# Optimization experiments

Hardware: AMD Instinct MI355X
Metric: run time of the kernel (lower is better)

Reference implementation:

```python
import jax, jax.numpy as jnp
import numpy as np

D1, D2 = 64, 64          # degree1, degree2
BW1, BW2 = 3, 3          # bandwidths
WIDTH = 64


def dst_mat(n):
    # Orthonormal DST-I matrix: self-inverse, stand-in for sp.WSWA / sp.sin_transform.
    k = np.arange(1, n + 1)
    M = np.sqrt(2.0 / (n + 1)) * np.sin(np.pi * np.outer(k, k) / (n + 1))
    return jnp.asarray(M, jnp.float32)


def transform2d(x, S_row, S_col):
    # apply spectral transform along last axis then axis -2 (T_pipe with axes [-1,-2])
    x = jnp.einsum('bcij,jk->bcik', x, S_col)
    return jnp.einsum('ki,bcij->bckj', S_row, x)


def wswano(u, w, out_ch):
    # WSWANO.forward: transform -> quasi-diag (unfold+einsum) multiply -> zero-pad -> inverse transform
    B, C, Nx, Ny = u.shape
    S1, S2 = dst_mat(Ny), dst_mat(Nx)
    a = transform2d(u, S2, S1)
    ap = a[:, :, :D1 + BW1 - 1, :D2 + BW2 - 1]
    # torch.nn.Unfold(kernel=(bw1,bw2)): patches ordered (c, ki, kj) x row-major positions
    patches = jnp.stack([ap[:, :, i:i + D1, j:j + D2]
                         for i in range(BW1) for j in range(BW2)], axis=2)  # [B,C,bw1*bw2,D1,D2]
    xp = patches.reshape(B, C * BW1 * BW2, D1 * D2)
    out = jnp.einsum('bix,iox->box', xp, w)  # quasi-diagonal spectral multiply
    b = jnp.zeros((B, out_ch, Nx, Ny), u.dtype).at[:, :, :D1, :D2].set(
        out.reshape(B, out_ch, D1, D2))
    return transform2d(b, S2, S1)  # DST-I is self-inverse => iT_pipe


def conv1x1(x, w, b):
    return jnp.einsum('bchw,oc->bohw', x, w) + b[None, :, None, None]


def gelu(x):
    return jax.nn.gelu(x, approximate=False)


def setup_inputs():
    key = jax.random.key(0)
    ks = jax.random.split(key, 18)
    B, Nx, Ny, W = 16, 128, 128, WIDTH

    def cw(k, cin, cout):
        return (2.0 / (cin + cout)) * jax.random.uniform(
            k, (cin * BW1 * BW2, cout, D1 * D2), jnp.float32)

    return {
        'x': jax.random.normal(ks[0], (B, Nx, Ny, 3), jnp.float32),
        'convl_w': cw(ks[1], 3, W - 3),
        'conv0_w': cw(ks[2], W, W),
        'conv1_w': cw(ks[3], W, W),
        'conv2_w': cw(ks[4], W, W),
        'conv3_w': cw(ks[5], W, W),
        'w0_w': 0.02 * jax.random.normal(ks[6], (W, W), jnp.float32),
        'w0_b': 0.02 * jax.random.normal(ks[7], (W,), jnp.float32),
        'w1_w': 0.02 * jax.random.normal(ks[8], (W, W), jnp.float32),
        'w1_b': 0.02 * jax.random.normal(ks[9], (W,), jnp.float32),
        'w2_w': 0.02 * jax.random.normal(ks[10], (W, W), jnp.float32),
        'w2_b': 0.02 * jax.random.normal(ks[11], (W,), jnp.float32),
        'w3_w': 0.02 * jax.random.normal(ks[12], (W, W), jnp.float32),
        'w3_b': 0.02 * jax.random.normal(ks[13], (W,), jnp.float32),
        'fc1_w': 0.02 * jax.random.normal(ks[14], (W, 128), jnp.float32),
        'fc1_b': 0.02 * jax.random.normal(ks[15], (128,), jnp.float32),
        'fc2_w': 0.02 * jax.random.normal(ks[16], (128, 1), jnp.float32),
        'fc2_b': 0.02 * jax.random.normal(ks[17], (1,), jnp.float32),
    }


def reference(x, convl_w, conv0_w, conv1_w, conv2_w, conv3_w,
              w0_w, w0_b, w1_w, w1_b, w2_w, w2_b, w3_w, w3_b,
              fc1_w, fc1_b, fc2_w, fc2_b):
    x = jnp.transpose(x, (0, 3, 1, 2))                       # [B,3,Nx,Ny]
    x = jnp.concatenate([x, gelu(wswano(x, convl_w, WIDTH - 3))], axis=1)
    for ww, wb, cw_ in ((w0_w, w0_b, conv0_w), (w1_w, w1_b, conv1_w),
                        (w2_w, w2_b, conv2_w), (w3_w, w3_b, conv3_w)):
        x = x + gelu(conv1x1(x, ww, wb) + wswano(x, cw_, WIDTH))  # skip + GELU block
    x = jnp.transpose(x, (0, 2, 3, 1))                       # [B,Nx,Ny,width]
    x = gelu(x @ fc1_w + fc1_b)
    return x @ fc2_w + fc2_b                                  # [B,Nx,Ny,1]
```

## Files before the change

kernel.cpp:

```cpp
#include <hip/hip_runtime.h>
#include <math.h>

#define NB 16
#define NN 128
#define WC 64
#define DD 64
#define NP 66

typedef float v4f __attribute__((ext_vector_type(4)));
typedef unsigned int u32;

__device__ __forceinline__ float gelu_f(float x) {
    return 0.5f * x * (1.0f + erff(x * 0.70710678118654752f));
}

__device__ __forceinline__ void gload16(const float* g, float* l) {
    __builtin_amdgcn_global_load_lds(
        (const __attribute__((address_space(1))) u32*)g,
        (__attribute__((address_space(3))) u32*)l, 16, 0, 0);
}

__global__ void k_dst(float* __restrict__ S) {
    int idx = blockIdx.x * 256 + threadIdx.x;
    int k = idx >> 7, j = idx & 127;
    double arg = 3.14159265358979323846 * (double)((k + 1) * (j + 1)) / 129.0;
    S[idx] = (float)(sqrt(2.0 / 129.0) * sin(arg));
}

__global__ void k_tin(const float* __restrict__ in, float* __restrict__ xc) {
    int idx = blockIdx.x * 256 + threadIdx.x;
    int j = idx & 127;
    int i = (idx >> 7) & 127;
    int t = idx >> 14;
    int b = t / 3, c = t - b * 3;
    xc[(((size_t)b * WC + c) << 14) + i * 128 + j] =
        in[((size_t)(b * 128 + i) * 128 + j) * 3 + c];
}

__global__ __launch_bounds__(256) void k_tfwd66(const float* __restrict__ Xg,
                                                float* __restrict__ Yc,
                                                const float* __restrict__ Sg,
                                                int Cact) {
    __shared__ float sSt[80 * 132];
    __shared__ float sU[66 * 132];
    int bid = blockIdx.x;
    int b = bid / Cact, c = bid - b * Cact;
    const float* X = Xg + (((size_t)b * WC + c) << 14);
    int tid = threadIdx.x;
    int tx = tid & 15, ty = tid >> 4;
    for (int l = tid; l < 80 * 128; l += 256)
        sSt[(l >> 7) * 132 + (l & 127)] = Sg[l];
    float acc[8][5];
#pragma unroll
    for (int r = 0; r < 8; ++r)
#pragma unroll
        for (int q = 0; q < 5; ++q) acc[r][q] = 0.f;
    for (int jh = 0; jh < 2; ++jh) {
        __syncthreads();
        for (int l = tid; l < 8192; l += 256)
            sU[(l >> 6) * 68 + (l & 63)] = X[((l >> 6) << 7) + jh * 64 + (l & 63)];
        __syncthreads();
        for (int jj = 0; jj < 64; jj += 4) {
            float4 xv[8], sv[5];
#pragma unroll
            for (int r = 0; r < 8; ++r)
                xv[r] = *(const float4*)&sU[(ty + 16 * r) * 68 + jj];
#pragma unroll
            for (int q = 0; q < 5; ++q)
                sv[q] = *(const float4*)&sSt[(tx + 16 * q) * 132 + jh * 64 + jj];
#pragma unroll
            for (int r = 0; r < 8; ++r)
#pragma unroll
                for (int q = 0; q < 5; ++q) {
                    acc[r][q] += xv[r].x * sv[q].x;
                    acc[r][q] += xv[r].y * sv[q].y;
                    acc[r][q] += xv[r].z * sv[q].z;
                    acc[r][q] += xv[r].w * sv[q].w;
                }
        }
    }
    __syncthreads();
#pragma unroll
    for (int q = 0; q < 5; ++q) {
        int k = tx + 16 * q;
        if (k < 66) {
#pragma unroll
            for (int r = 0; r < 8; ++r)
                sU[k * 132 + ty + 16 * r] = acc[r][q];
        }
    }
    __syncthreads();
    float a2[5][5];
#pragma unroll
    for (int r = 0; r < 5; ++r)
#pragma unroll
        for (int q = 0; q < 5; ++q) a2[r][q] = 0.f;
    for (int i0 = 0; i0 < 128; i0 += 4) {
        float4 sv[5], tv[5];
#pragma unroll
        for (int r = 0; r < 5; ++r)
            sv[r] = *(const float4*)&sSt[(ty + 16 * r) * 132 + i0];
#pragma unroll
        for (int q = 0; q < 5; ++q) {
            int m = tx + 16 * q;
            if (m < 66) tv[q] = *(const float4*)&sU[m * 132 + i0];
            else { tv[q].x = 0.f; tv[q].y = 0.f; tv[q].z = 0.f; tv[q].w = 0.f; }
        }
#pragma unroll
        for (int r = 0; r < 5; ++r)
#pragma unroll
            for (int q = 0; q < 5; ++q) {
                a2[r][q] += sv[r].x * tv[q].x;
                a2[r][q] += sv[r].y * tv[q].y;
                a2[r][q] += sv[r].z * tv[q].z;
                a2[r][q] += sv[r].w * tv[q].w;
            }
    }
    float* Y = Yc + (size_t)(b * WC + c) * 4488;
#pragma unroll
    for (int r = 0; r < 5; ++r) {
        int kk = ty + 16 * r;
        if (kk < 66) {
#pragma unroll
            for (int q = 0; q < 5; ++q) {
                int m = tx + 16 * q;
                if (m < 66) Y[kk * 68 + m] = a2[r][q];
            }
        }
    }
}

__global__ __launch_bounds__(256, 3) void k_tinv(const float* __restrict__ Op,
                                                 float* __restrict__ Yg,
                                                 const float* __restrict__ Sg,
                                                 int Cact, int ncc, int ch_off, int do_gelu) {
    __shared__ float sS[64 * 64];
    __shared__ float sXT[64 * 132];
    int bid = blockIdx.x;
    int b = bid / Cact, c = bid - b * Cact;
    const float* X = Op + ((size_t)(b * WC + c) << 12);
    const size_t cstride = (size_t)NB * WC * 4096;
    float* Y = Yg + (((size_t)b * WC + c + ch_off) << 14);
    int tid = threadIdx.x;
    for (int l = tid; l < 4096; l += 256)
        sS[l] = Sg[((l >> 6) << 7) + (l & 63)];
    for (int l = tid; l < 4096; l += 256) {
        int r = l >> 6, q = l & 63;
        float v = X[l];
        for (int cc = 1; cc < ncc; ++cc) v += X[cc * cstride + l];
        sXT[r * 66 + q] = v;
    }
    __syncthreads();
    int cg = tid & 7;
    int rg = tid >> 3;
    v4f aP[2][2], aM[2][2];
#pragma unroll
    for (int r = 0; r < 2; ++r)
#pragma unroll
        for (int m = 0; m < 2; ++m) {
            aP[r][m].x = 0.f; aP[r][m].y = 0.f; aP[r][m].z = 0.f; aP[r][m].w = 0.f;
            aM[r][m].x = 0.f; aM[r][m].y = 0.f; aM[r][m].z = 0.f; aM[r][m].w = 0.f;
        }
    for (int jp = 0; jp < 32; ++jp) {
        float2 x0 = *(const float2*)&sXT[(rg * 2 + 0) * 66 + 2 * jp];
        float2 x1 = *(const float2*)&sXT[(rg * 2 + 1) * 66 + 2 * jp];
#pragma unroll
        for (int m = 0; m < 2; ++m) {
            v4f se = *(const v4f*)&sS[(2 * jp) * 64 + cg * 4 + 32 * m];
            v4f so = *(const v4f*)&sS[(2 * jp + 1) * 64 + cg * 4 + 32 * m];
            aP[0][m] += se * x0.x;  aM[0][m] += so * x0.y;
            aP[1][m] += se * x1.x;  aM[1][m] += so * x1.y;
        }
    }
    __syncthreads();
#pragma unroll
    for (int r = 0; r < 2; ++r)
#pragma unroll
        for (int m = 0; m < 2; ++m) {
            v4f tlo = aP[r][m] + aM[r][m];
            v4f td  = aP[r][m] - aM[r][m];
            v4f thi; thi.x = td.w; thi.y = td.z; thi.z = td.y; thi.w = td.x;
            int row = rg * 2 + r;
            *(v4f*)&sXT[row * 132 + cg * 4 + 32 * m] = tlo;
            *(v4f*)&sXT[row * 132 + 124 - cg * 4 - 32 * m] = thi;
        }
    __syncthreads();
    v4f p2[2][4], m2[2][4];
#pragma unroll
    for (int r = 0; r < 2; ++r)
#pragma unroll
        for (int m = 0; m < 4; ++m) {
            p2[r][m].x = 0.f; p2[r][m].y = 0.f; p2[r][m].z = 0.f; p2[r][m].w = 0.f;
            m2[r][m].x = 0.f; m2[r][m].y = 0.f; m2[r][m].z = 0.f; m2[r][m].w = 0.f;
        }
    for (int ip = 0; ip < 32; ++ip) {
        float2 sve = *(const float2*)&sS[(2 * ip) * 64 + rg * 2];
        float2 svo = *(const float2*)&sS[(2 * ip + 1) * 64 + rg * 2];
#pragma unroll
        for (int m = 0; m < 4; ++m) {
            v4f te = *(const v4f*)&sXT[(2 * ip) * 132 + cg * 4 + 32 * m];
            v4f to = *(const v4f*)&sXT[(2 * ip + 1) * 132 + cg * 4 + 32 * m];
            p2[0][m] += te * sve.x;  p2[1][m] += te * sve.y;
            m2[0][m] += to * svo.x;  m2[1][m] += to * svo.y;
        }
    }
#pragma unroll
    for (int r = 0; r < 2; ++r) {
        int rlo = rg * 2 + r, rhi = 127 - rlo;
#pragma unroll
        for (int m = 0; m < 4; ++m) {
            v4f ylo = p2[r][m] + m2[r][m];
            v4f yhi = p2[r][m] - m2[r][m];
            if (do_gelu) {
                ylo.x = gelu_f(ylo.x); ylo.y = gelu_f(ylo.y);
                ylo.z = gelu_f(ylo.z); ylo.w = gelu_f(ylo.w);
                yhi.x = gelu_f(yhi.x); yhi.y = gelu_f(yhi.y);
                yhi.z = gelu_f(yhi.z); yhi.w = gelu_f(yhi.w);
            }
            *(v4f*)&Y[rlo * 128 + cg * 4 + 32 * m] = ylo;
            *(v4f*)&Y[rhi * 128 + cg * 4 + 32 * m] = yhi;
        }
    }
}

__global__ __launch_bounds__(256, 2) void k_mix6(const float* __restrict__ Ac,
                                                 const float* __restrict__ Wt,
                                                 float* __restrict__ Op,
                                                 int Cin, int Cout, int cper) {
    __shared__ __align__(16) float sa[2][16 * 4 * 68];
    int bx = blockIdx.x;
    int ocb = blockIdx.y;
    int ccb = blockIdx.z;
    int c0 = ccb * cper;
    int c1 = c0 + cper; if (c1 > Cin) c1 = Cin;
    int tid = threadIdx.x;
    int ocl = tid & 7, yq = (tid >> 3) & 15, xh = tid >> 7;
    int x = bx * 2 + xh;
    int oc = ocb * 8 + ocl;
    bool ocok = oc < Cout;
    v4f z4; z4.x = 0.f; z4.y = 0.f; z4.z = 0.f; z4.w = 0.f;

    const size_t wstep = (size_t)Cout * 4096;
    const float* wbase = Wt + (size_t)(ocok ? oc : 0) * 4096 + x * 64 + (yq << 2);

    int gbase[5];
#pragma unroll
    for (int k = 0; k < 5; ++k) {
        int f = 4 * tid + 1024 * k;
        int fv = (f < 4352) ? f : 0;
        int bb = fv / 272; int off = fv - bb * 272;
        gbase[k] = bb * (WC * 4488) + bx * 136 + off;
    }

    float acc[16][4];
#pragma unroll
    for (int bb = 0; bb < 16; ++bb)
#pragma unroll
        for (int k = 0; k < 4; ++k) acc[bb][k] = 0.f;

    {
        const float* src = Ac + (size_t)c0 * 4488;
#pragma unroll
        for (int k = 0; k < 4; ++k)
            gload16(src + gbase[k], &sa[0][4 * tid + 1024 * k]);
        if (tid < 64) gload16(src + gbase[4], &sa[0][4 * tid + 4096]);
    }
    v4f wvA[9];
#pragma unroll
    for (int t = 0; t < 9; ++t)
        wvA[t] = ocok ? __builtin_nontemporal_load(
                            (const v4f*)(wbase + ((size_t)c0 * 9 + t) * wstep))
                      : z4;
    __syncthreads();

    int cur = 0;
    for (int c = c0; c < c1; ++c) {
        bool hn = (c + 1) < c1;
        v4f wvN[9];
        if (hn) {
            float* dst = sa[cur ^ 1];
            const float* src = Ac + (size_t)(c + 1) * 4488;
#pragma unroll
            for (int k = 0; k < 4; ++k)
                gload16(src + gbase[k], dst + 4 * tid + 1024 * k);
            if (tid < 64) gload16(src + gbase[4], dst + 4 * tid + 4096);
#pragma unroll
            for (int t = 0; t < 9; ++t)
                wvN[t] = ocok ? __builtin_nontemporal_load(
                                    (const v4f*)(wbase + ((size_t)(c + 1) * 9 + t) * wstep))
                              : z4;
        }
        const float* sab = sa[cur];
#pragma unroll
        for (int pi = 0; pi < 3; ++pi) {
#pragma unroll
            for (int bb = 0; bb < 16; ++bb) {
                const float* sp = &sab[(bb * 4 + xh + pi) * 68 + (yq << 2)];
                float4 s0 = *(const float4*)sp;
                float2 s1 = *(const float2*)(sp + 4);
                float sv[6] = {s0.x, s0.y, s0.z, s0.w, s1.x, s1.y};
#pragma unroll
                for (int k = 0; k < 4; ++k)
#pragma unroll
                    for (int pj = 0; pj < 3; ++pj)
                        acc[bb][k] = fmaf(sv[k + pj], wvA[pi * 3 + pj][k], acc[bb][k]);
            }
        }
        if (hn) {
            __syncthreads();
#pragma unroll
            for (int t = 0; t < 9; ++t) wvA[t] = wvN[t];
            cur ^= 1;
        }
    }

    if (ocok) {
        float* Opc = Op + (size_t)ccb * ((size_t)NB * WC * 4096);
#pragma unroll
        for (int bb = 0; bb < 16; ++bb) {
            float4 o4;
            o4.x = acc[bb][0]; o4.y = acc[bb][1];
            o4.z = acc[bb][2]; o4.w = acc[bb][3];
            *(float4*)&Opc[(((size_t)bb * WC + oc) << 12) + x * 64 + (yq << 2)] = o4;
        }
    }
}

__global__ __launch_bounds__(256) void k_blockup(float* __restrict__ xc,
                                                 const float* __restrict__ sp,
                                                 const float* __restrict__ wmat,
                                                 const float* __restrict__ bias) {
    __shared__ float sw[64 * 64];
    __shared__ float sx[128 * 65];
    __shared__ float sb[64];
    int bi = blockIdx.x;
    int b = bi >> 7, i = bi & 127;
    int tid = threadIdx.x;
    for (int l = tid; l < 4096; l += 256) sw[l] = wmat[l];
    if (tid < 64) sb[tid] = bias[tid];
    for (int l = tid; l < 8192; l += 256) {
        int c = l >> 7, j = l & 127;
        sx[j * 65 + c] = xc[(((size_t)b * WC + c) << 14) + i * 128 + j];
    }
    __syncthreads();
    int j = tid & 127, h = tid >> 7;
    float xr[64];
#pragma unroll
    for (int c = 0; c < 64; ++c) xr[c] = sx[j * 65 + c];
#pragma unroll 2
    for (int o = 0; o < 32; ++o) {
        int oc = h * 32 + o;
        float a = sb[oc];
#pragma unroll
        for (int c4 = 0; c4 < 16; ++c4) {
            v4f w4 = *(const v4f*)&sw[oc * 64 + c4 * 4];
            a = fmaf(xr[c4 * 4 + 0], w4.x, a);
            a = fmaf(xr[c4 * 4 + 1], w4.y, a);
            a = fmaf(xr[c4 * 4 + 2], w4.z, a);
            a = fmaf(xr[c4 * 4 + 3], w4.w, a);
        }
        size_t gi = (((size_t)b * WC + oc) << 14) + i * 128 + j;
        float v = a + sp[gi];
        xc[gi] = sx[j * 65 + oc] + gelu_f(v);
    }
}

__global__ __launch_bounds__(256) void k_fc(const float* __restrict__ xc,
                                            const float* __restrict__ W1,
                                            const float* __restrict__ b1,
                                            const float* __restrict__ W2,
                                            const float* __restrict__ b2,
                                            float* __restrict__ out) {
    __shared__ float sW1T[128 * 68];
    __shared__ float sx[128 * 65];
    __shared__ float sW2[128];
    __shared__ float sb1[128];
    __shared__ float spart[256];
    int bi = blockIdx.x; int b = bi >> 7, i = bi & 127;
    int tid = threadIdx.x;
    for (int l = tid; l < 8192; l += 256) {
        int c = l >> 7, oo = l & 127;
        sW1T[oo * 68 + c] = W1[l];
    }
    if (tid < 128) { sW2[tid] = W2[tid]; sb1[tid] = b1[tid]; }
    for (int l = tid; l < 8192; l += 256) {
        int c = l >> 7, j = l & 127;
        sx[j * 65 + c] = xc[(((size_t)b * WC + c) << 14) + i * 128 + j];
    }
    __syncthreads();
    int j = tid & 127, h = tid >> 7;
    float xr[64];
#pragma unroll
    for (int c = 0; c < 64; ++c) xr[c] = sx[j * 65 + c];
    float part = 0.f;
#pragma unroll 2
    for (int o = 0; o < 64; ++o) {
        int oo = h * 64 + o;
        float a = sb1[oo];
#pragma unroll
        for (int c4 = 0; c4 < 16; ++c4) {
            v4f w4 = *(const v4f*)&sW1T[oo * 68 + c4 * 4];
            a = fmaf(xr[c4 * 4 + 0], w4.x, a);
            a = fmaf(xr[c4 * 4 + 1], w4.y, a);
            a = fmaf(xr[c4 * 4 + 2], w4.z, a);
            a = fmaf(xr[c4 * 4 + 3], w4.w, a);
        }
        part += gelu_f(a) * sW2[oo];
    }
    spart[j * 2 + h] = part;
    __syncthreads();
    if (h == 0) out[(size_t)bi * 128 + j] = spart[j * 2] + spart[j * 2 + 1] + b2[0];
}

extern "C" void kernel_launch(void* const* d_in, const int* in_sizes, int n_in,
                              void* d_out, int out_size, void* d_ws, size_t ws_size,
                              hipStream_t stream) {
    (void)in_sizes; (void)n_in; (void)out_size; (void)ws_size;
    const float* x_in    = (const float*)d_in[0];
    const float* convl_w = (const float*)d_in[1];
    const float* conv_w[4] = {(const float*)d_in[2], (const float*)d_in[3],
                              (const float*)d_in[4], (const float*)d_in[5]};
    const float* ww[4] = {(const float*)d_in[6], (const float*)d_in[8],
                          (const float*)d_in[10], (const float*)d_in[12]};
    const float* wb[4] = {(const float*)d_in[7], (const float*)d_in[9],
                          (const float*)d_in[11], (const float*)d_in[13]};
    const float* fc1w = (const float*)d_in[14];
    const float* fc1b = (const float*)d_in[15];
    const float* fc2w = (const float*)d_in[16];
    const float* fc2b = (const float*)d_in[17];
    float* out = (float*)d_out;

    float* S   = (float*)d_ws;
    float* xc  = S + 16384;
    float* t1  = xc + (size_t)NB * WC * 16384;
    float* tA  = t1 + (size_t)NB * WC * 16384;
    float* Op  = tA + (size_t)NB * WC * 4488;

    k_dst<<<64, 256, 0, stream>>>(S);
    k_tin<<<3072, 256, 0, stream>>>(x_in, xc);

    k_tfwd66<<<NB * 3, 256, 0, stream>>>(xc, tA, S, 3);
    k_mix6<<<dim3(32, 8, 1), 256, 0, stream>>>(tA, convl_w, Op, 3, 61, 3);
    k_tinv<<<NB * 61, 256, 0, stream>>>(Op, xc, S, 61, 1, 3, 1);

    for (int L = 0; L < 4; ++L) {
        k_tfwd66<<<NB * WC, 256, 0, stream>>>(xc, tA, S, WC);
        k_mix6<<<dim3(32, 8, 2), 256, 0, stream>>>(tA, conv_w[L], Op, WC, WC, 32);
        k_tinv<<<NB * WC, 256, 0, stream>>>(Op, t1, S, WC, 2, 0, 0);
        k_blockup<<<2048, 256, 0, stream>>>(xc, t1, ww[L], wb[L]);
    }

    k_fc<<<2048, 256, 0, stream>>>(xc, fc1w, fc1b, fc2w, fc2b, out);
}
```

Measured before the change: 1.606 ms.

## Exploit DST-I row symmetry to halve forward transform contraction length

```diff
diff --git a/kernel.cpp b/kernel.cpp
--- a/kernel.cpp
+++ b/kernel.cpp
@@ -37,39 +37,51 @@
         in[((size_t)(b * 128 + i) * 128 + j) * 3 + c];
 }
 
-__global__ __launch_bounds__(256) void k_tfwd66(const float* __restrict__ Xg,
-                                                float* __restrict__ Yc,
-                                                const float* __restrict__ Sg,
-                                                int Cact) {
-    __shared__ float sSt[80 * 132];
-    __shared__ float sU[66 * 132];
+__global__ __launch_bounds__(256, 1) void k_tfwd66(const float* __restrict__ Xg,
+                                                   float* __restrict__ Yc,
+                                                   const float* __restrict__ Sg,
+                                                   int Cact) {
+    __shared__ float sS[66 * 68];
+    __shared__ float sXe[64 * 68];
+    __shared__ float sXo[64 * 68];
+    __shared__ float sTe[66 * 68];
+    __shared__ float sTo[66 * 68];
     int bid = blockIdx.x;
     int b = bid / Cact, c = bid - b * Cact;
     const float* X = Xg + (((size_t)b * WC + c) << 14);
     int tid = threadIdx.x;
     int tx = tid & 15, ty = tid >> 4;
-    for (int l = tid; l < 80 * 128; l += 256)
-        sSt[(l >> 7) * 132 + (l & 127)] = Sg[l];
-    float acc[8][5];
-#pragma unroll
-    for (int r = 0; r < 8; ++r)
-#pragma unroll
-        for (int q = 0; q < 5; ++q) acc[r][q] = 0.f;
-    for (int jh = 0; jh < 2; ++jh) {
+    for (int l = tid; l < 66 * 64; l += 256)
+        sS[(l >> 6) * 68 + (l & 63)] = Sg[((l >> 6) << 7) + (l & 63)];
+    const float* xb = (tx & 1) ? sXo : sXe;
+    for (int h = 0; h < 2; ++h) {
         __syncthreads();
-        for (int l = tid; l < 8192; l += 256)
-            sU[(l >> 6) * 68 + (l & 63)] = X[((l >> 6) << 7) + jh * 64 + (l & 63)];
+        for (int l = tid; l < 4096; l += 256) {
+            int row = l >> 6, j = l & 63;
+            const float* xr = X + ((h * 64 + row) << 7);
+            float x0 = xr[j], x1 = xr[127 - j];
+            sXe[row * 68 + j] = x0 + x1;
+            sXo[row * 68 + j] = x0 - x1;
+        }
         __syncthreads();
+        float acc[4][5];
+#pragma unroll
+        for (int r = 0; r < 4; ++r)
+#pragma unroll
+            for (int q = 0; q < 5; ++q) acc[r][q] = 0.f;
         for (int jj = 0; jj < 64; jj += 4) {
-            float4 xv[8], sv[5];
-#pragma unroll
-            for (int r = 0; r < 8; ++r)
-                xv[r] = *(const float4*)&sU[(ty + 16 * r) * 68 + jj];
-#pragma unroll
-            for (int q = 0; q < 5; ++q)
-                sv[q] = *(const float4*)&sSt[(tx + 16 * q) * 132 + jh * 64 + jj];
-#pragma unroll
-            for (int r = 0; r < 8; ++r)
+            float4 xv[4], sv[5];
+#pragma unroll
+            for (int r = 0; r < 4; ++r)
+                xv[r] = *(const float4*)&xb[(ty + 16 * r) * 68 + jj];
+#pragma unroll
+            for (int q = 0; q < 5; ++q) {
+                int k = tx + 16 * q;
+                int kc = (k < 66) ? k : 65;
+                sv[q] = *(const float4*)&sS[kc * 68 + jj];
+            }
+#pragma unroll
+            for (int r = 0; r < 4; ++r)
 #pragma unroll
                 for (int q = 0; q < 5; ++q) {
                     acc[r][q] += xv[r].x * sv[q].x;
@@ -78,33 +90,56 @@
                     acc[r][q] += xv[r].w * sv[q].w;
                 }
         }
-    }
-    __syncthreads();
-#pragma unroll
-    for (int q = 0; q < 5; ++q) {
-        int k = tx + 16 * q;
-        if (k < 66) {
-#pragma unroll
-            for (int r = 0; r < 8; ++r)
-                sU[k * 132 + ty + 16 * r] = acc[r][q];
-        }
-    }
-    __syncthreads();
+        if (h == 0) {
+#pragma unroll
+            for (int q = 0; q < 5; ++q) {
+                int k = tx + 16 * q;
+                if (k < 66) {
+#pragma unroll
+                    for (int r = 0; r < 4; ++r) {
+                        int i = ty + 16 * r;
+                        float v = acc[r][q];
+                        sTe[k * 68 + i] = v;
+                        sTo[k * 68 + i] = v;
+                    }
+                }
+            }
+        } else {
+#pragma unroll
+            for (int q = 0; q < 5; ++q) {
+                int k = tx + 16 * q;
+                if (k < 66) {
+#pragma unroll
+                    for (int r = 0; r < 4; ++r) {
+                        int i = 63 - (ty + 16 * r);
+                        float v = acc[r][q];
+                        sTe[k * 68 + i] += v;
+                        sTo[k * 68 + i] -= v;
+                    }
+                }
+            }
+        }
+    }
+    __syncthreads();
+    const float* tb = (ty & 1) ? sTo : sTe;
     float a2[5][5];
 #pragma unroll
     for (int r = 0; r < 5; ++r)
 #pragma unroll
         for (int q = 0; q < 5; ++q) a2[r][q] = 0.f;
-    for (int i0 = 0; i0 < 128; i0 += 4) {
+    for (int i0 = 0; i0 < 64; i0 += 4) {
         float4 sv[5], tv[5];
 #pragma unroll
-        for (int r = 0; r < 5; ++r)
-            sv[r] = *(const float4*)&sSt[(ty + 16 * r) * 132 + i0];
+        for (int r = 0; r < 5; ++r) {
+            int kk = ty + 16 * r;
+            int kc = (kk < 66) ? kk : 65;
+            sv[r] = *(const float4*)&sS[kc * 68 + i0];
+        }
 #pragma unroll
         for (int q = 0; q < 5; ++q) {
             int m = tx + 16 * q;
-            if (m < 66) tv[q] = *(const float4*)&sU[m * 132 + i0];
-            else { tv[q].x = 0.f; tv[q].y = 0.f; tv[q].z = 0.f; tv[q].w = 0.f; }
+            int mc = (m < 66) ? m : 65;
+            tv[q] = *(const float4*)&tb[mc * 68 + i0];
         }
 #pragma unroll
         for (int r = 0; r < 5; ++r)
```

New measurement: 1.538 ms. -4.2%, faster.
